# Kernel tuning notes

Hardware: AMD Instinct MI355X
Metric: run time of the kernel (lower is better)

The kernel has to match this reference:

```python
import jax, jax.numpy as jnp
import numpy as np

B, N, D = 8192, 49, 3
D3 = 42  # embed_dim // 3
E = 128
K = 3    # min(3, N-1) nearest neighbors for local density


def setup_inputs() -> dict:
    key = jax.random.key(0)
    ks = jax.random.split(key, 8)
    points = jax.random.normal(ks[0], (B, N, D), jnp.float32)
    return {
        "points": points,
        "W_dist": jax.random.normal(ks[1], (1, D3), jnp.float32) * 1.0,
        "b_dist": jnp.zeros((D3,), jnp.float32),
        "emb": jax.random.normal(ks[2], (50, D3), jnp.float32) * 0.02,
        "W_den": jax.random.normal(ks[3], (1, D3), jnp.float32) * 1.0,
        "b_den": jnp.zeros((D3,), jnp.float32),
        "W_out": jax.random.normal(ks[4], (3 * D3, E), jnp.float32) * (1.0 / np.sqrt(3 * D3)),
        "b_out": jnp.zeros((E,), jnp.float32),
    }


def _local_density(points):
    # Batched cdist with diagonal masked to +inf, then mean of K smallest dists.
    sq = jnp.sum(points * points, axis=-1)                      # [B,N]
    d2 = sq[:, :, None] + sq[:, None, :] \
         - 2.0 * jnp.einsum('bnd,bmd->bnm', points, points)      # [B,N,N]
    d2 = jnp.maximum(d2, 0.0)
    eye = jnp.eye(points.shape[1], dtype=bool)
    d2 = jnp.where(eye, jnp.inf, d2)
    dists = jnp.sqrt(d2)
    nearest = -jax.lax.top_k(-dists, K)[0]                      # [B,N,K] smallest
    return jnp.mean(nearest, axis=-1, keepdims=True)            # [B,N,1]


def reference(points, W_dist, b_dist, emb, W_den, b_den, W_out, b_out):
    b, n, _ = points.shape
    centroid = jnp.mean(points, axis=1, keepdims=True)          # [B,1,3]
    rel = points - centroid
    centroid_dist = jnp.linalg.norm(rel, axis=-1, keepdims=True)  # [B,N,1]
    dist_f = centroid_dist @ W_dist + b_dist                    # [B,N,D3]
    # n_valid == N (no mask), a constant index into the count embedding
    count_f = jnp.broadcast_to(emb[n][None, None, :], (b, n, emb.shape[1]))
    density = _local_density(points)                            # [B,N,1]
    den_f = density @ W_den + b_den                             # [B,N,D3]
    features = jnp.concatenate([dist_f, count_f, den_f], axis=-1)  # [B,N,3*D3]
    return features @ W_out + b_out                             # [B,N,E]
```

## Files before the change

### kernel.cpp

```cpp
#include <hip/hip_runtime.h>
#include <math.h>

#define N_     49
#define D3_    42
#define E_     128
#define WPB    4
#define ROUNDS 2


#define KNN(W, CD, DN) do {                                                  \
    const int n = (lane < N_) ? lane : N_ - 1;                               \
    const float px = pts[W][3*n], py = pts[W][3*n+1], pz = pts[W][3*n+2];    \
    float sx = 0.f, sy = 0.f, sz = 0.f;                                      \
    float t0 = INFINITY, t1 = INFINITY, t2 = INFINITY;                       \
    for (int m = 0; m < N_; ++m) {                                           \
        float qx = pts[W][3*m], qy = pts[W][3*m+1], qz = pts[W][3*m+2];      \
        sx += qx; sy += qy; sz += qz;                                        \
        float dx = px - qx, dy = py - qy, dz = pz - qz;                      \
        float d2 = fmaf(dx, dx, fmaf(dy, dy, dz * dz));                      \
        if (m != n) {                                                        \
            if (d2 < t0)      { t2 = t1; t1 = t0; t0 = d2; }                 \
            else if (d2 < t1) { t2 = t1; t1 = d2; }                          \
            else if (d2 < t2) { t2 = d2; }                                   \
        }                                                                    \
    }                                                                        \
    const float inv = 1.0f / (float)N_;                                      \
    float cx = sx*inv, cy = sy*inv, cz = sz*inv;                             \
    float ex = px-cx, ey = py-cy, ez = pz-cz;                                \
    CD = sqrtf(fmaf(ex, ex, fmaf(ey, ey, ez * ez)));                         \
    DN = (sqrtf(t0) + sqrtf(t1) + sqrtf(t2)) * (1.0f / 3.0f);                \
} while (0)

#define STORES(BB, CD, DN) do {                                              \
    float4* ob = out4 + (long long)(BB) * (N_ * 32);                         \
    _Pragma("unroll")                                                        \
    for (int j = 0; j < 25; ++j) {                                           \
        int row = 2*j + (lane >> 5);                                         \
        float a = __shfl(CD, row);                                           \
        float d = __shfl(DN, row);                                           \
        if (row < N_) {                                                      \
            float4 r;                                                        \
            r.x = fmaf(a, u4.x, fmaf(d, v4.x, c4.x));                        \
            r.y = fmaf(a, u4.y, fmaf(d, v4.y, c4.y));                        \
            r.z = fmaf(a, u4.z, fmaf(d, v4.z, c4.z));                        \
            r.w = fmaf(a, u4.w, fmaf(d, v4.w, c4.w));                        \
            ob[row * 32 + q] = r;                                            \
        }                                                                    \
    }                                                                        \
} while (0)

__global__ __launch_bounds__(256) void fused_all(
        const float* __restrict__ points,
        const float* __restrict__ W_dist,
        const float* __restrict__ b_dist,
        const float* __restrict__ emb,
        const float* __restrict__ W_den,
        const float* __restrict__ b_den,
        const float* __restrict__ W_out,
        const float* __restrict__ b_out,
        float4* __restrict__ out4,
        int B) {
    __shared__ float pts[WPB][N_ * 3];
    __shared__ __align__(16) float sUVC[3 * E_];

    const int tid    = threadIdx.x;
    const int lane   = tid & 63;
    const int w      = tid >> 6;
    const int nwaves = gridDim.x * WPB;
    const int wid    = blockIdx.x * WPB + w;

    const long long b0 = wid;
    const bool v0 = (b0 < B);
    float s0a = 0.f, s0b = 0.f, s0c = 0.f;
    if (v0) {
        const float* pb = points + b0 * (N_ * 3);
        s0a = pb[lane];
        s0b = pb[64 + lane];
        if (lane < N_ * 3 - 128) s0c = pb[128 + lane];
    }

    if (tid < E_) {
        const float* embN = emb + N_ * D3_;
        float u = 0.f, vv = 0.f, c = b_out[tid];
        for (int j = 0; j < D3_; ++j) {
            float w0 = W_out[j * E_ + tid];
            float w1 = W_out[(D3_ + j) * E_ + tid];
            float w2 = W_out[(2 * D3_ + j) * E_ + tid];
            u  = fmaf(W_dist[j], w0, u);
            vv = fmaf(W_den[j],  w2, vv);
            c  = fmaf(b_dist[j], w0, c);
            c  = fmaf(embN[j],   w1, c);
            c  = fmaf(b_den[j],  w2, c);
        }
        sUVC[tid]          = u;
        sUVC[E_ + tid]     = vv;
        sUVC[2 * E_ + tid] = c;
    }

    if (v0) {
        pts[w][lane]      = s0a;
        pts[w][64 + lane] = s0b;
        if (lane < N_ * 3 - 128) pts[w][128 + lane] = s0c;
    }

    const long long b1 = (long long)wid + nwaves;
    const bool v1 = (b1 < B);
    float s1a = 0.f, s1b = 0.f, s1c = 0.f;
    if (v1) {
        const float* pb = points + b1 * (N_ * 3);
        s1a = pb[lane];
        s1b = pb[64 + lane];
        if (lane < N_ * 3 - 128) s1c = pb[128 + lane];
    }

    float cd0 = 0.f, dn0 = 0.f;
    if (v0) { KNN(w, cd0, dn0); }

    __syncthreads();
    const int q = lane & 31;
    const float4 u4 = *(const float4*)&sUVC[4 * q];
    const float4 v4 = *(const float4*)&sUVC[E_ + 4 * q];
    const float4 c4 = *(const float4*)&sUVC[2 * E_ + 4 * q];

    if (v0) { STORES(b0, cd0, dn0); }

    if (v1) {
        pts[w][lane]      = s1a;
        pts[w][64 + lane] = s1b;
        if (lane < N_ * 3 - 128) pts[w][128 + lane] = s1c;
        float cd1, dn1;
        KNN(w, cd1, dn1);
        STORES(b1, cd1, dn1);
    }
}

extern "C" void kernel_launch(void* const* d_in, const int* in_sizes, int n_in,
                              void* d_out, int out_size, void* d_ws, size_t ws_size,
                              hipStream_t stream) {
    const float* points = (const float*)d_in[0];
    const float* W_dist = (const float*)d_in[1];
    const float* b_dist = (const float*)d_in[2];
    const float* emb    = (const float*)d_in[3];
    const float* W_den  = (const float*)d_in[4];
    const float* b_den  = (const float*)d_in[5];
    const float* W_out  = (const float*)d_in[6];
    const float* b_out  = (const float*)d_in[7];

    const int B = in_sizes[0] / (N_ * 3);
    const int nblocks = (B + WPB * ROUNDS - 1) / (WPB * ROUNDS);

    fused_all<<<nblocks, 64 * WPB, 0, stream>>>(
        points, W_dist, b_dist, emb, W_den, b_den, W_out, b_out,
        (float4*)d_out, B);
}
```

Before: 226.6 us.

## Process one batch per wave and store points as padded float4 in LDS

Drops the two-round per-wave loop so each wave handles a single batch element, doubling the grid size. Each lane now loads its own point directly and writes it to LDS as a padded float4, so the inner KNN loop reads one vector LDS load per neighbour instead of three scalar loads. More blocks means the per-block weight precompute (the W_out reduction into sUVC) runs twice as often, and the load of the second batch element no longer overlaps with compute. The lane-strided 3-float global loads are less coalesced than the previous contiguous loads.

Result: no change. 227.2 us, median of 2 (+0.3%).

```diff
diff --git a/kernel.cpp b/kernel.cpp
--- a/kernel.cpp
+++ b/kernel.cpp
@@ -5,49 +5,7 @@
 #define D3_    42
 #define E_     128
 #define WPB    4
-#define ROUNDS 2
 
-
-#define KNN(W, CD, DN) do {                                                  \
-    const int n = (lane < N_) ? lane : N_ - 1;                               \
-    const float px = pts[W][3*n], py = pts[W][3*n+1], pz = pts[W][3*n+2];    \
-    float sx = 0.f, sy = 0.f, sz = 0.f;                                      \
-    float t0 = INFINITY, t1 = INFINITY, t2 = INFINITY;                       \
-    for (int m = 0; m < N_; ++m) {                                           \
-        float qx = pts[W][3*m], qy = pts[W][3*m+1], qz = pts[W][3*m+2];      \
-        sx += qx; sy += qy; sz += qz;                                        \
-        float dx = px - qx, dy = py - qy, dz = pz - qz;                      \
-        float d2 = fmaf(dx, dx, fmaf(dy, dy, dz * dz));                      \
-        if (m != n) {                                                        \
-            if (d2 < t0)      { t2 = t1; t1 = t0; t0 = d2; }                 \
-            else if (d2 < t1) { t2 = t1; t1 = d2; }                          \
-            else if (d2 < t2) { t2 = d2; }                                   \
-        }                                                                    \
-    }                                                                        \
-    const float inv = 1.0f / (float)N_;                                      \
-    float cx = sx*inv, cy = sy*inv, cz = sz*inv;                             \
-    float ex = px-cx, ey = py-cy, ez = pz-cz;                                \
-    CD = sqrtf(fmaf(ex, ex, fmaf(ey, ey, ez * ez)));                         \
-    DN = (sqrtf(t0) + sqrtf(t1) + sqrtf(t2)) * (1.0f / 3.0f);                \
-} while (0)
-
-#define STORES(BB, CD, DN) do {                                              \
-    float4* ob = out4 + (long long)(BB) * (N_ * 32);                         \
-    _Pragma("unroll")                                                        \
-    for (int j = 0; j < 25; ++j) {                                           \
-        int row = 2*j + (lane >> 5);                                         \
-        float a = __shfl(CD, row);                                           \
-        float d = __shfl(DN, row);                                           \
-        if (row < N_) {                                                      \
-            float4 r;                                                        \
-            r.x = fmaf(a, u4.x, fmaf(d, v4.x, c4.x));                        \
-            r.y = fmaf(a, u4.y, fmaf(d, v4.y, c4.y));                        \
-            r.z = fmaf(a, u4.z, fmaf(d, v4.z, c4.z));                        \
-            r.w = fmaf(a, u4.w, fmaf(d, v4.w, c4.w));                        \
-            ob[row * 32 + q] = r;                                            \
-        }                                                                    \
-    }                                                                        \
-} while (0)
 
 __global__ __launch_bounds__(256) void fused_all(
         const float* __restrict__ points,
@@ -60,23 +18,20 @@
         const float* __restrict__ b_out,
         float4* __restrict__ out4,
         int B) {
-    __shared__ float pts[WPB][N_ * 3];
+    __shared__ float4 pts4[WPB][N_];
     __shared__ __align__(16) float sUVC[3 * E_];
 
-    const int tid    = threadIdx.x;
-    const int lane   = tid & 63;
-    const int w      = tid >> 6;
-    const int nwaves = gridDim.x * WPB;
-    const int wid    = blockIdx.x * WPB + w;
+    const int tid  = threadIdx.x;
+    const int lane = tid & 63;
+    const int w    = tid >> 6;
+    const int wid  = blockIdx.x * WPB + w;
+    const bool v0  = (wid < B);
 
-    const long long b0 = wid;
-    const bool v0 = (b0 < B);
-    float s0a = 0.f, s0b = 0.f, s0c = 0.f;
+    const int n = (lane < N_) ? lane : N_ - 1;
+    float px = 0.f, py = 0.f, pz = 0.f;
     if (v0) {
-        const float* pb = points + b0 * (N_ * 3);
-        s0a = pb[lane];
-        s0b = pb[64 + lane];
-        if (lane < N_ * 3 - 128) s0c = pb[128 + lane];
+        const float* pb = points + (long long)wid * (N_ * 3) + 3 * n;
+        px = pb[0]; py = pb[1]; pz = pb[2];
     }
 
     if (tid < E_) {
@@ -97,24 +52,31 @@
         sUVC[2 * E_ + tid] = c;
     }
 
-    if (v0) {
-        pts[w][lane]      = s0a;
-        pts[w][64 + lane] = s0b;
-        if (lane < N_ * 3 - 128) pts[w][128 + lane] = s0c;
+    if (v0 && lane < N_) {
+        pts4[w][lane] = make_float4(px, py, pz, 0.f);
     }
 
-    const long long b1 = (long long)wid + nwaves;
-    const bool v1 = (b1 < B);
-    float s1a = 0.f, s1b = 0.f, s1c = 0.f;
-    if (v1) {
-        const float* pb = points + b1 * (N_ * 3);
-        s1a = pb[lane];
-        s1b = pb[64 + lane];
-        if (lane < N_ * 3 - 128) s1c = pb[128 + lane];
+    float cd = 0.f, dn = 0.f;
+    if (v0) {
+        float sx = 0.f, sy = 0.f, sz = 0.f;
+        float t0 = INFINITY, t1 = INFINITY, t2 = INFINITY;
+        for (int m = 0; m < N_; ++m) {
+            float4 qq = pts4[w][m];
+            sx += qq.x; sy += qq.y; sz += qq.z;
+            float dx = px - qq.x, dy = py - qq.y, dz = pz - qq.z;
+            float d2 = fmaf(dx, dx, fmaf(dy, dy, dz * dz));
+            if (m != n) {
+                if (d2 < t0)      { t2 = t1; t1 = t0; t0 = d2; }
+                else if (d2 < t1) { t2 = t1; t1 = d2; }
+                else if (d2 < t2) { t2 = d2; }
+            }
+        }
+        const float inv = 1.0f / (float)N_;
+        float cx = sx * inv, cy = sy * inv, cz = sz * inv;
+        float ex = px - cx, ey = py - cy, ez = pz - cz;
+        cd = sqrtf(fmaf(ex, ex, fmaf(ey, ey, ez * ez)));
+        dn = (sqrtf(t0) + sqrtf(t1) + sqrtf(t2)) * (1.0f / 3.0f);
     }
-
-    float cd0 = 0.f, dn0 = 0.f;
-    if (v0) { KNN(w, cd0, dn0); }
 
     __syncthreads();
     const int q = lane & 31;
@@ -122,15 +84,22 @@
     const float4 v4 = *(const float4*)&sUVC[E_ + 4 * q];
     const float4 c4 = *(const float4*)&sUVC[2 * E_ + 4 * q];
 
-    if (v0) { STORES(b0, cd0, dn0); }
-
-    if (v1) {
-        pts[w][lane]      = s1a;
-        pts[w][64 + lane] = s1b;
-        if (lane < N_ * 3 - 128) pts[w][128 + lane] = s1c;
-        float cd1, dn1;
-        KNN(w, cd1, dn1);
-        STORES(b1, cd1, dn1);
+    if (v0) {
+        float4* ob = out4 + (long long)wid * (N_ * 32);
+#pragma unroll
+        for (int j = 0; j < 25; ++j) {
+            int row = 2 * j + (lane >> 5);
+            float a = __shfl(cd, row);
+            float d = __shfl(dn, row);
+            if (row < N_) {
+                float4 r;
+                r.x = fmaf(a, u4.x, fmaf(d, v4.x, c4.x));
+                r.y = fmaf(a, u4.y, fmaf(d, v4.y, c4.y));
+                r.z = fmaf(a, u4.z, fmaf(d, v4.z, c4.z));
+                r.w = fmaf(a, u4.w, fmaf(d, v4.w, c4.w));
+                ob[row * 32 + q] = r;
+            }
+        }
     }
 }
 
@@ -147,7 +116,7 @@
     const float* b_out  = (const float*)d_in[7];
 
     const int B = in_sizes[0] / (N_ * 3);
-    const int nblocks = (B + WPB * ROUNDS - 1) / (WPB * ROUNDS);
+    const int nblocks = (B + WPB - 1) / WPB;
 
     fused_all<<<nblocks, 64 * WPB, 0, stream>>>(
         points, W_dist, b_dist, emb, W_den, b_den, W_out, b_out,
```
